# Performance work log

Hardware: AMD Instinct MI355X
Metric: run time of the kernel (lower is better)

The kernel has to match this reference:

```python
import jax, jax.numpy as jnp
import numpy as np

EPS = 1e-5

def layer_norm(x, g, b):
    m = jnp.mean(x, axis=-1, keepdims=True)
    v = jnp.var(x, axis=-1, keepdims=True)
    return (x - m) / jnp.sqrt(v + EPS) * g + b

def setup_inputs() -> dict:
    key = jax.random.key(0)
    B, N, D, H, F = 2, 2048, 1024, 16, 4096
    ks = jax.random.split(key, 12)
    s = 0.02
    return {
        "x": jax.random.normal(ks[0], (B, N, D), dtype=jnp.float32),
        "wq": jax.random.normal(ks[1], (D, D), dtype=jnp.float32) * s,
        "bq": jnp.zeros((D,), jnp.float32),
        "wk": jax.random.normal(ks[2], (D, D), dtype=jnp.float32) * s,
        "bk": jnp.zeros((D,), jnp.float32),
        "wv": jax.random.normal(ks[3], (D, D), dtype=jnp.float32) * s,
        "bv": jnp.zeros((D,), jnp.float32),
        "g1": jnp.ones((D,), jnp.float32),
        "b1": jnp.zeros((D,), jnp.float32),
        "g2": jnp.ones((D,), jnp.float32),
        "b2": jnp.zeros((D,), jnp.float32),
        "w1": jax.random.normal(ks[4], (D, F), dtype=jnp.float32) * s,
        "bw1": jnp.zeros((F,), jnp.float32),
        "gf": jnp.ones((F,), jnp.float32),
        "bf": jnp.zeros((F,), jnp.float32),
        "w2": jax.random.normal(ks[5], (F, D), dtype=jnp.float32) * s,
        "bw2": jnp.zeros((D,), jnp.float32),
        "num_heads": 16,
    }

def reference(x, wq, bq, wk, bk, wv, bv, g1, b1, g2, b2, w1, bw1, gf, bf, w2, bw2, num_heads):
    B, N, D = x.shape
    H = num_heads
    E = D // H
    h = layer_norm(x, g1, b1)
    q = (h @ wq + bq).reshape(B, N, H, E).transpose(0, 2, 1, 3)  # B H N E
    k = (h @ wk + bk).reshape(B, N, H, E).transpose(0, 2, 1, 3)
    v = (h @ wv + bv).reshape(B, N, H, E).transpose(0, 2, 1, 3)
    # NOTE: original scales by 1/sqrt(1/emb_dim) == sqrt(emb_dim)
    scale = jnp.sqrt(jnp.float32(D))
    score = jnp.einsum('bhne,bhme->bhnm', q, k) * scale  # B H N N
    w = jax.nn.softmax(score, axis=-1)
    attn = jnp.einsum('bhnm,bhme->bhne', w, v)
    attn = attn.transpose(0, 2, 1, 3).reshape(B, N, D)
    x = x + attn  # dropout = identity in eval
    h2 = layer_norm(x, g2, b2)
    # MLP: Linear -> (Dropout) -> LayerNorm -> ReLU -> Linear; NO residual add (faithful to source)
    u = layer_norm(h2 @ w1 + bw1, gf, bf)
    return jax.nn.relu(u) @ w2 + bw2
```

## Files before the change

### kernel.cpp

```cpp
#include <hip/hip_runtime.h>

typedef unsigned short u16;
typedef _Float16 f16;
typedef _Float16 f16x8 __attribute__((ext_vector_type(8)));
typedef float f32x4 __attribute__((ext_vector_type(4)));
typedef unsigned short u16x4 __attribute__((ext_vector_type(4)));
typedef unsigned int u32x4 __attribute__((ext_vector_type(4)));

__device__ __forceinline__ u16 f2h(float f) {
    f16 h = (f16)f;
    return *reinterpret_cast<u16*>(&h);
}
__device__ __forceinline__ float h2f(u16 u) {
    f16 h = *reinterpret_cast<f16*>(&u);
    return (float)h;
}

__device__ __forceinline__ float exp2v(float x) { return __builtin_amdgcn_exp2f(x); }

__device__ __forceinline__ unsigned cvtpkh(float lo, float hi) {
    unsigned r;
    asm("v_cvt_pkrtz_f16_f32 %0, %1, %2" : "=v"(r) : "v"(lo), "v"(hi));
    return r;
}

__device__ __forceinline__ void gload16(const u16* g, u16* l) {
    __builtin_amdgcn_global_load_lds((const __attribute__((address_space(1))) unsigned int*)g,
                                     (__attribute__((address_space(3))) unsigned int*)l, 16, 0, 0);
}

#define RAW_BARRIER() __builtin_amdgcn_s_barrier()
#define WAITCNT_VM(N) asm volatile("s_waitcnt vmcnt(" #N ")" ::: "memory")

__device__ __forceinline__ int xcd_swz(int bid, int nwg) {
    return (bid & 7) * (nwg >> 3) + (bid >> 3);
}

__global__ void transpose_cast3(const float* __restrict__ W0, u16* __restrict__ T0,
                                const float* __restrict__ W1, u16* __restrict__ T1,
                                const float* __restrict__ W2, u16* __restrict__ T2,
                                int K, int N) {
    __shared__ float t[32][33];
    const float* W = (blockIdx.z == 0) ? W0 : (blockIdx.z == 1) ? W1 : W2;
    u16* Wt = (blockIdx.z == 0) ? T0 : (blockIdx.z == 1) ? T1 : T2;
    const int n0 = blockIdx.x * 32, k0 = blockIdx.y * 32;
    const int tx = threadIdx.x, ty = threadIdx.y;
#pragma unroll
    for (int i = 0; i < 32; i += 8)
        t[ty + i][tx] = W[(size_t)(k0 + ty + i) * N + n0 + tx];
    __syncthreads();
#pragma unroll
    for (int i = 0; i < 32; i += 8)
        Wt[(size_t)(n0 + ty + i) * K + k0 + tx] = f2h(t[tx][ty + i]);
}

__global__ void transpose_cast(const float* __restrict__ W, u16* __restrict__ Wt,
                               int K, int N) {
    __shared__ float t[32][33];
    const int n0 = blockIdx.x * 32, k0 = blockIdx.y * 32;
    const int tx = threadIdx.x, ty = threadIdx.y;
#pragma unroll
    for (int i = 0; i < 32; i += 8)
        t[ty + i][tx] = W[(size_t)(k0 + ty + i) * N + n0 + tx];
    __syncthreads();
#pragma unroll
    for (int i = 0; i < 32; i += 8)
        Wt[(size_t)(n0 + ty + i) * K + k0 + tx] = f2h(t[tx][ty + i]);
}

__global__ __launch_bounds__(256) void ln_f32_f16(const float* __restrict__ in,
                                                  const float* __restrict__ g,
                                                  const float* __restrict__ b,
                                                  u16* __restrict__ out) {
    constexpr int Dl = 1024;
    const int row = blockIdx.x, tid = threadIdx.x;
    const float4 v = *(const float4*)&in[(size_t)row * Dl + tid * 4];
    const float* vp = (const float*)&v;
    float s = v.x + v.y + v.z + v.w;
    float s2 = v.x * v.x + v.y * v.y + v.z * v.z + v.w * v.w;
#pragma unroll
    for (int off = 32; off; off >>= 1) { s += __shfl_xor(s, off); s2 += __shfl_xor(s2, off); }
    __shared__ float red[8];
    const int lane = tid & 63, wid = tid >> 6;
    if (lane == 0) { red[wid] = s; red[4 + wid] = s2; }
    __syncthreads();
    s = red[0] + red[1] + red[2] + red[3];
    s2 = red[4] + red[5] + red[6] + red[7];
    const float mean = s * (1.0f / Dl);
    const float rstd = rsqrtf(s2 * (1.0f / Dl) - mean * mean + 1e-5f);
    u16x4 pk;
#pragma unroll
    for (int i = 0; i < 4; ++i) {
        const int col = tid * 4 + i;
        pk[i] = f2h((vp[i] - mean) * rstd * g[col] + b[col]);
    }
    *(u16x4*)&out[(size_t)row * Dl + tid * 4] = pk;
}

__global__ __launch_bounds__(256) void ln_relu_f16(u16* __restrict__ mid,
                                                   const float* __restrict__ g,
                                                   const float* __restrict__ b) {
    constexpr int Fl = 4096;
    const int row = blockIdx.x, tid = threadIdx.x;
    u16* rp = mid + (size_t)row * Fl;
    float v[16];
    u32x4 raw[2];
#pragma unroll
    for (int c = 0; c < 2; ++c) raw[c] = *(const u32x4*)&rp[tid * 16 + c * 8];
#pragma unroll
    for (int c = 0; c < 2; ++c)
#pragma unroll
        for (int j = 0; j < 4; ++j) {
            const unsigned u = raw[c][j];
            v[c * 8 + j * 2] = h2f((u16)(u & 0xffffu));
            v[c * 8 + j * 2 + 1] = h2f((u16)(u >> 16));
        }
    float s = 0.f, s2 = 0.f;
#pragma unroll
    for (int i = 0; i < 16; ++i) { s += v[i]; s2 += v[i] * v[i]; }
#pragma unroll
    for (int off = 32; off; off >>= 1) { s += __shfl_xor(s, off); s2 += __shfl_xor(s2, off); }
    __shared__ float red[8];
    const int lane = tid & 63, wid = tid >> 6;
    if (lane == 0) { red[wid] = s; red[4 + wid] = s2; }
    __syncthreads();
    s = red[0] + red[1] + red[2] + red[3];
    s2 = red[4] + red[5] + red[6] + red[7];
    const float mean = s * (1.0f / Fl);
    const float rstd = rsqrtf(s2 * (1.0f / Fl) - mean * mean + 1e-5f);
    unsigned w[8];
#pragma unroll
    for (int j = 0; j < 8; ++j) {
        const int col = tid * 16 + j * 2;
        const float y0 = fmaxf((v[j * 2] - mean) * rstd * g[col] + b[col], 0.f);
        const float y1 = fmaxf((v[j * 2 + 1] - mean) * rstd * g[col + 1] + b[col + 1], 0.f);
        w[j] = (unsigned)f2h(y0) | ((unsigned)f2h(y1) << 16);
    }
    *(u32x4*)&rp[tid * 16] = *(u32x4*)&w[0];
    *(u32x4*)&rp[tid * 16 + 8] = *(u32x4*)&w[4];
}

template <int EPI, int BN>
__global__ __launch_bounds__(256, 2) void gemm_f16(const u16* __restrict__ A,
                                                   const u16* __restrict__ Bt,
                                                   const float* __restrict__ bias,
                                                   u16* __restrict__ outB,
                                                   float* __restrict__ outF,
                                                   int M_, int N_, int K_) {
    constexpr int BK = 32;
    constexpr int NJ = BN / 32;
    __shared__ u16 As[2][128 * BK];
    __shared__ u16 Bs[2][BN * BK];
    const int tid = threadIdx.x;
    const int lane = tid & 63;
    const int wid = tid >> 6;
    const int nM = gridDim.y;
    const int swz = xcd_swz(blockIdx.y * gridDim.x + blockIdx.x, gridDim.x * gridDim.y);
    const int m0 = (swz % nM) * 128;
    const int n0 = (swz / nM) * BN;
    const int wr = (wid >> 1) * 64;
    const int wc = (wid & 1) * (BN / 2);
    const int fr = lane & 15;
    const int fg = (lane >> 4) * 8;

    const int srow = wid * 32 + (lane >> 2);
    const int srB = wid * (BN / 4) + (lane >> 2);
    const int scol = (lane & 3) * 8;
    const u16* pa0 = A + (size_t)(m0 + srow) * K_ + scol;
    const u16* pa1 = pa0 + (size_t)16 * K_;
    const u16* pb0 = Bt + (size_t)(n0 + srB) * K_ + scol;
    const u16* pb1 = pb0 + (size_t)16 * K_;
    const int aoff = wid * 1024;
    const int boff = wid * (BN / 4) * BK;

    auto stage = [&](int k0, int buf) {
        gload16(pa0 + k0, &As[buf][aoff]);
        gload16(pa1 + k0, &As[buf][aoff + 512]);
        gload16(pb0 + k0, &Bs[buf][boff]);
        if constexpr (BN == 128) gload16(pb1 + k0, &Bs[buf][boff + 512]);
    };

    f32x4 acc[4][NJ] = {};
    const int nt = K_ / BK;

    stage(0, 0);
    WAITCNT_VM(0);
    RAW_BARRIER();

    for (int t = 0; t < nt; ++t) {
        const int buf = t & 1;
        if (t + 1 < nt) stage((t + 1) * BK, buf ^ 1);
        f16x8 aF[4], bF[NJ];
#pragma unroll
        for (int i = 0; i < 4; ++i) aF[i] = *(const f16x8*)&As[buf][(wr + i * 16 + fr) * BK + fg];
#pragma unroll
        for (int j = 0; j < NJ; ++j) bF[j] = *(const f16x8*)&Bs[buf][(wc + j * 16 + fr) * BK + fg];
#pragma unroll
        for (int i = 0; i < 4; ++i)
#pragma unroll
            for (int j = 0; j < NJ; ++j)
                acc[i][j] = __builtin_amdgcn_mfma_f32_16x16x32_f16(aF[i], bF[j], acc[i][j], 0, 0, 0);
        WAITCNT_VM(0);
        RAW_BARRIER();
    }

    const int g4 = (lane >> 4) * 4;
#pragma unroll
    for (int i = 0; i < 4; ++i) {
#pragma unroll
        for (int j = 0; j < NJ; ++j) {
            const int mb = m0 + wr + i * 16 + g4;
            const int nb = n0 + wc + j * 16 + fr;
            const float bv = bias[nb];
#pragma unroll
            for (int r = 0; r < 4; ++r)
                outB[(size_t)(mb + r) * N_ + nb] = f2h(acc[i][j][r] + bv);
        }
    }
}

__global__ __launch_bounds__(256, 4) void gemm_f16_splitk(const u16* __restrict__ A,
                                                          const u16* __restrict__ Bt,
                                                          float* __restrict__ p0,
                                                          float* __restrict__ p1,
                                                          int M_, int N_, int K_) {
    constexpr int BK = 32, BN = 64;
    __shared__ u16 As[2][128 * BK];
    __shared__ u16 Bs[2][BN * BK];
    const int tid = threadIdx.x;
    const int lane = tid & 63;
    const int wid = tid >> 6;
    const int nM = gridDim.y;
    const int swz = xcd_swz(blockIdx.y * gridDim.x + blockIdx.x, gridDim.x * gridDim.y);
    const int m0 = (swz % nM) * 128;
    const int n0 = (swz / nM) * BN;
    const int kBase = blockIdx.z * (K_ >> 1);
    float* dst = blockIdx.z ? p1 : p0;
    const int wr = (wid >> 1) * 64;
    const int wc = (wid & 1) * (BN / 2);
    const int fr = lane & 15;
    const int fg = (lane >> 4) * 8;

    const int srow = wid * 32 + (lane >> 2);
    const int srB = wid * (BN / 4) + (lane >> 2);
    const int scol = (lane & 3) * 8;
    const u16* pa0 = A + (size_t)(m0 + srow) * K_ + kBase + scol;
    const u16* pa1 = pa0 + (size_t)16 * K_;
    const u16* pb0 = Bt + (size_t)(n0 + srB) * K_ + kBase + scol;
    const u16* pb1 = pb0 + (size_t)16 * K_;
    const int aoff = wid * 1024;
    const int boff = wid * (BN / 4) * BK;

    auto stage = [&](int k0, int buf) {
        gload16(pa0 + k0, &As[buf][aoff]);
        gload16(pa1 + k0, &As[buf][aoff + 512]);
        gload16(pb0 + k0, &Bs[buf][boff]);
    };

    f32x4 acc[4][2] = {};
    const int nt = (K_ >> 1) / BK;

    stage(0, 0);
    WAITCNT_VM(0);
    RAW_BARRIER();

    for (int t = 0; t < nt; ++t) {
        const int buf = t & 1;
        if (t + 1 < nt) stage((t + 1) * BK, buf ^ 1);
        f16x8 aF[4], bF[2];
#pragma unroll
        for (int i = 0; i < 4; ++i) aF[i] = *(const f16x8*)&As[buf][(wr + i * 16 + fr) * BK + fg];
#pragma unroll
        for (int j = 0; j < 2; ++j) bF[j] = *(const f16x8*)&Bs[buf][(wc + j * 16 + fr) * BK + fg];
#pragma unroll
        for (int i = 0; i < 4; ++i)
#pragma unroll
            for (int j = 0; j < 2; ++j)
                acc[i][j] = __builtin_amdgcn_mfma_f32_16x16x32_f16(aF[i], bF[j], acc[i][j], 0, 0, 0);
        WAITCNT_VM(0);
        RAW_BARRIER();
    }

    const int g4 = (lane >> 4) * 4;
#pragma unroll
    for (int i = 0; i < 4; ++i)
#pragma unroll
        for (int j = 0; j < 2; ++j) {
            const int mb = m0 + wr + i * 16 + g4;
            const int nb = n0 + wc + j * 16 + fr;
#pragma unroll
            for (int r = 0; r < 4; ++r)
                dst[(size_t)(mb + r) * N_ + nb] = acc[i][j][r];
        }
}

__global__ __launch_bounds__(256) void reduce2_bias(const float* __restrict__ p0,
                                                    const float* __restrict__ p1,
                                                    const float* __restrict__ bias,
                                                    float* __restrict__ out, int N_) {
    const size_t i4 = (size_t)blockIdx.x * 256 + threadIdx.x;
    const float4 a = ((const float4*)p0)[i4];
    const float4 b = ((const float4*)p1)[i4];
    const int col4 = (int)(i4 % (N_ / 4));
    const float4 bi = ((const float4*)bias)[col4];
    float4 o;
    o.x = a.x + b.x + bi.x;
    o.y = a.y + b.y + bi.y;
    o.z = a.z + b.z + bi.z;
    o.w = a.w + b.w + bi.w;
    ((float4*)out)[i4] = o;
}

__global__ __launch_bounds__(256, 4) void gemm_qkv(const u16* __restrict__ A,
                                                   const u16* __restrict__ qW,
                                                   const u16* __restrict__ kW,
                                                   const u16* __restrict__ vW,
                                                   const float* __restrict__ bq,
                                                   const float* __restrict__ bk,
                                                   const float* __restrict__ bv,
                                                   u16* __restrict__ qb, u16* __restrict__ kb,
                                                   u16* __restrict__ vtb,
                                                   int M_, int K_) {
    constexpr int BK = 32;
    __shared__ u16 As[2][128 * BK];
    __shared__ u16 Bs[2][64 * BK];
    const int tid = threadIdx.x;
    const int lane = tid & 63;
    const int wid = tid >> 6;
    const int nM = gridDim.y;
    const int swz = xcd_swz(blockIdx.y * gridDim.x + blockIdx.x, gridDim.x * gridDim.y);
    const int m0 = (swz % nM) * 128;
    const int bx = swz / nM;
    const int region = bx >> 4;
    const int n0 = (bx & 15) * 64;
    const int wr = (wid >> 1) * 64;
    const int wc = (wid & 1) * 32;
    const int fr = lane & 15;
    const int fg = (lane >> 4) * 8;

    const int srow = wid * 32 + (lane >> 2);
    const int srB = wid * 16 + (lane >> 2);
    const int scol = (lane & 3) * 8;

    const u16* B = (region == 0) ? qW : (region == 1) ? kW : vW;
    const u16* pa0 = A + (size_t)(m0 + srow) * K_ + scol;
    const u16* pa1 = pa0 + (size_t)16 * K_;
    const u16* pb = B + (size_t)(n0 + srB) * K_ + scol;
    const int aoff = wid * 1024;
    const int boff = wid * 512;

    auto stage = [&](int k0, int buf) {
        gload16(pa0 + k0, &As[buf][aoff]);
        gload16(pa1 + k0, &As[buf][aoff + 512]);
        gload16(pb + k0, &Bs[buf][boff]);
    };

    f32x4 acc[4][2] = {};
    const int nt = K_ / BK;

    stage(0, 0);
    WAITCNT_VM(0);
    RAW_BARRIER();

    for (int t = 0; t < nt; ++t) {
        const int buf = t & 1;
        if (t + 1 < nt) stage((t + 1) * BK, buf ^ 1);
        f16x8 aF[4], bF[2];
#pragma unroll
        for (int i = 0; i < 4; ++i) aF[i] = *(const f16x8*)&As[buf][(wr + i * 16 + fr) * BK + fg];
#pragma unroll
        for (int j = 0; j < 2; ++j) bF[j] = *(const f16x8*)&Bs[buf][(wc + j * 16 + fr) * BK + fg];
#pragma unroll
        for (int i = 0; i < 4; ++i)
#pragma unroll
            for (int j = 0; j < 2; ++j)
                acc[i][j] = __builtin_amdgcn_mfma_f32_16x16x32_f16(aF[i], bF[j], acc[i][j], 0, 0, 0);
        WAITCNT_VM(0);
        RAW_BARRIER();
    }

    const float* bias = (region == 0) ? bq : (region == 1) ? bk : bv;
    const float scale = (region == 0) ? 32.f : 1.f;
    const int g4 = (lane >> 4) * 4;
#pragma unroll
    for (int i = 0; i < 4; ++i) {
#pragma unroll
        for (int j = 0; j < 2; ++j) {
            const int mb = m0 + wr + i * 16 + g4;
            const int nb = n0 + wc + j * 16 + fr;
            const float bv_ = bias[nb];
            const int h = nb >> 6, e = nb & 63;
            if (region < 2) {
                u16* outp = (region == 0) ? qb : kb;
#pragma unroll
                for (int r = 0; r < 4; ++r) {
                    const int m = mb + r;
                    const size_t idx = ((size_t)((m >> 11) * 16 + h) * 2048 + (m & 2047)) * 64 + e;
                    outp[idx] = f2h((acc[i][j][r] + bv_) * scale);
                }
            } else {
                const int b_ = mb >> 11, np = mb & 2047;
                u16x4 pk;
#pragma unroll
                for (int r = 0; r < 4; ++r) pk[r] = f2h(acc[i][j][r] + bv_);
                *(u16x4*)&vtb[((size_t)(b_ * 16 + h) * 64 + e) * 2048 + np] = pk;
            }
        }
    }
}

__global__ __launch_bounds__(512, 4) void attn_kernel(const u16* __restrict__ q,
                                                      const u16* __restrict__ k,
                                                      const u16* __restrict__ vt,
                                                      const float* __restrict__ x,
                                                      float* __restrict__ x2) {
    constexpr int N = 2048, E = 64, KB = 64, NT = N / KB;
    constexpr float L2E = 1.4426950408889634f;
    __shared__ u16 Ks[2][64 * 64];
    __shared__ u16 Vs[2][64 * 64];
    __shared__ unsigned Ps[8][16][36];

    const int tid = threadIdx.x;
    const int lane = tid & 63;
    const int wid = tid >> 6;
    const int swzb = xcd_swz(blockIdx.x, gridDim.x);
    const int bh = swzb >> 4;
    const int q0 = (swzb & 15) * 128;
    const u16* qh = q + (size_t)bh * N * E;
    const u16* kh = k + (size_t)bh * N * E;
    const u16* vh = vt + (size_t)bh * E * N;

    const int fr = lane & 15;
    const int fgrp = lane >> 4;
    const int fg8 = fgrp * 8;
    int pc[2];
#pragma unroll
    for (int ks = 0; ks < 2; ++ks) pc[ks] = 8 * (((ks << 2) + fgrp) ^ (fr & 7));

    const int srow = wid * 8 + (lane >> 3);
    const int swc = 8 * ((lane & 7) ^ (lane >> 3));
    u16* dK = &Ks[0][wid * 8 * 64];
    u16* dV = &Vs[0][wid * 8 * 64];
    constexpr int BUFO = 64 * 64;

    f16x8 qf[2];
#pragma unroll
    for (int ks = 0; ks < 2; ++ks)
        qf[ks] = *(const f16x8*)&qh[(size_t)(q0 + wid * 16 + fr) * E + ks * 32 + fg8];

    auto stage = [&](int t, int buf) {
        const size_t kb = (size_t)t * KB;
        gload16(kh + (kb + srow) * E + swc, dK + buf * BUFO);
        gload16(vh + (size_t)srow * N + kb + swc, dV + buf * BUFO);
    };

    f32x4 o[4] = {};
    float mrow = -1e30f, lpart = 0.f;

    stage(0, 0);

    for (int t = 0; t < NT; ++t) {
        const int buf = t & 1;
        RAW_BARRIER();
        if (t + 1 < NT) {
            stage(t + 1, buf ^ 1);
            WAITCNT_VM(2);
        } else {
            WAITCNT_VM(0);
        }
        RAW_BARRIER();

        const u16* KK = &Ks[buf][0];
        const u16* VV = &Vs[buf][0];

        f32x4 s[4] = {};
        __builtin_amdgcn_s_setprio(1);
#pragma unroll
        for (int fn = 0; fn < 4; ++fn)
#pragma unroll
            for (int ks = 0; ks < 2; ++ks) {
                const f16x8 kf = *(const f16x8*)&KK[(fn * 16 + fr) * 64 + pc[ks]];
                s[fn] = __builtin_amdgcn_mfma_f32_16x16x32_f16(kf, qf[ks], s[fn], 0, 0, 0);
            }
        __builtin_amdgcn_s_setprio(0);

        float lmax = fmaxf(fmaxf(fmaxf(s[0][0], s[0][1]), fmaxf(s[0][2], s[0][3])),
                           fmaxf(fmaxf(s[1][0], s[1][1]), fmaxf(s[1][2], s[1][3])));
        lmax = fmaxf(lmax, fmaxf(fmaxf(fmaxf(s[2][0], s[2][1]), fmaxf(s[2][2], s[2][3])),
                                 fmaxf(fmaxf(s[3][0], s[3][1]), fmaxf(s[3][2], s[3][3]))));
        if (!__all(lmax <= mrow + 8.f)) {
            float m2 = fmaxf(lmax, __shfl_xor(lmax, 16));
            m2 = fmaxf(m2, __shfl_xor(m2, 32));
            const float mnew = fmaxf(mrow, m2);
            const float fac = exp2v((mrow - mnew) * L2E);
            mrow = mnew;
            lpart *= fac;
            float fo[4];
#pragma unroll
            for (int r = 0; r < 4; ++r) fo[r] = __shfl(fac, fgrp * 4 + r);
#pragma unroll
            for (int fe = 0; fe < 4; ++fe)
#pragma unroll
                for (int r = 0; r < 4; ++r) o[fe][r] *= fo[r];
        }

        const float nml = -mrow * L2E;
#pragma unroll
        for (int fn = 0; fn < 4; ++fn) {
            const float p0 = exp2v(fmaf(s[fn][0], L2E, nml));
            const float p1 = exp2v(fmaf(s[fn][1], L2E, nml));
            const float p2 = exp2v(fmaf(s[fn][2], L2E, nml));
            const float p3 = exp2v(fmaf(s[fn][3], L2E, nml));
            lpart += (p0 + p1) + (p2 + p3);
            uint2 w;
            w.x = cvtpkh(p0, p1);
            w.y = cvtpkh(p2, p3);
            *(uint2*)&Ps[wid][fr][fn * 8 + fgrp * 2] = w;
        }

        const u16* prow = (const u16*)&Ps[wid][fr][0];
        f16x8 pf[2];
#pragma unroll
        for (int ks = 0; ks < 2; ++ks) pf[ks] = *(const f16x8*)&prow[ks * 32 + fg8];
        __builtin_amdgcn_s_setprio(1);
#pragma unroll
        for (int fe = 0; fe < 4; ++fe)
#pragma unroll
            for (int ks = 0; ks < 2; ++ks) {
                const f16x8 vf = *(const f16x8*)&VV[(fe * 16 + fr) * 64 + pc[ks]];
                o[fe] = __builtin_amdgcn_mfma_f32_16x16x32_f16(pf[ks], vf, o[fe], 0, 0, 0);
            }
        __builtin_amdgcn_s_setprio(0);
    }

    float lsum = lpart + __shfl_xor(lpart, 16);
    lsum += __shfl_xor(lsum, 32);
    float rl[4];
#pragma unroll
    for (int r = 0; r < 4; ++r) rl[r] = 1.0f / __shfl(lsum, fgrp * 4 + r);

    const int b_ = bh >> 4, h_ = bh & 15;
#pragma unroll
    for (int fe = 0; fe < 4; ++fe)
#pragma unroll
        for (int r = 0; r < 4; ++r) {
            const int npos = q0 + wid * 16 + fgrp * 4 + r;
            const size_t idx = ((size_t)(b_ * 2048 + npos)) * 1024 + h_ * 64 + fe * 16 + fr;
            x2[idx] = x[idx] + o[fe][r] * rl[r];
        }
}

extern "C" void kernel_launch(void* const* d_in, const int* in_sizes, int n_in,
                              void* d_out, int out_size, void* d_ws, size_t ws_size,
                              hipStream_t stream) {
    const float* x = (const float*)d_in[0];
    const float* wq = (const float*)d_in[1];
    const float* bq = (const float*)d_in[2];
    const float* wk = (const float*)d_in[3];
    const float* bk = (const float*)d_in[4];
    const float* wv = (const float*)d_in[5];
    const float* bv = (const float*)d_in[6];
    const float* g1 = (const float*)d_in[7];
    const float* b1 = (const float*)d_in[8];
    const float* g2 = (const float*)d_in[9];
    const float* b2 = (const float*)d_in[10];
    const float* w1 = (const float*)d_in[11];
    const float* bw1 = (const float*)d_in[12];
    const float* gf = (const float*)d_in[13];
    const float* bf = (const float*)d_in[14];
    const float* w2 = (const float*)d_in[15];
    const float* bw2 = (const float*)d_in[16];
    float* out = (float*)d_out;

    constexpr int Bc = 2, Nc = 2048, Dc = 1024, Fc = 4096, Mc = 4096;

    char* ws = (char*)d_ws;
    auto alloc = [&](size_t bytes) {
        char* p = ws;
        ws += (bytes + 255) & ~(size_t)255;
        return p;
    };
    u16* wqt = (u16*)alloc((size_t)Dc * Dc * 2);
    u16* wkt = (u16*)alloc((size_t)Dc * Dc * 2);
    u16* wvt = (u16*)alloc((size_t)Dc * Dc * 2);
    u16* w1t = (u16*)alloc((size_t)Dc * Fc * 2);
    u16* w2t = (u16*)alloc((size_t)Fc * Dc * 2);
    char* region = (char*)alloc((size_t)Mc * Dc * 2 * 4);
    u16* h1 = (u16*)region;
    u16* qb = h1 + (size_t)Mc * Dc;
    u16* kb = qb + (size_t)Mc * Dc;
    u16* vtb = kb + (size_t)Mc * Dc;
    u16* mid = (u16*)region;
    float* x2 = (float*)alloc((size_t)Mc * Dc * 4);
    u16* h2 = (u16*)alloc((size_t)Mc * Dc * 2);
    float* p1 = (float*)alloc((size_t)Mc * Dc * 4);
    float* p0 = x2;

    const dim3 tb(32, 8);
    transpose_cast3<<<dim3(Dc / 32, Dc / 32, 3), tb, 0, stream>>>(wq, wqt, wk, wkt, wv, wvt, Dc, Dc);
    transpose_cast<<<dim3(Fc / 32, Dc / 32), tb, 0, stream>>>(w1, w1t, Dc, Fc);
    transpose_cast<<<dim3(Dc / 32, Fc / 32), tb, 0, stream>>>(w2, w2t, Fc, Dc);

    ln_f32_f16<<<Mc, 256, 0, stream>>>(x, g1, b1, h1);

    gemm_qkv<<<dim3(48, Mc / 128), 256, 0, stream>>>(h1, wqt, wkt, wvt, bq, bk, bv,
                                                     qb, kb, vtb, Mc, Dc);

    attn_kernel<<<Bc * 16 * (Nc / 128), 512, 0, stream>>>(qb, kb, vtb, x, x2);

    ln_f32_f16<<<Mc, 256, 0, stream>>>(x2, g2, b2, h2);

    gemm_f16<0, 128><<<dim3(Fc / 128, Mc / 128), 256, 0, stream>>>(h2, w1t, bw1, mid, nullptr, Mc, Fc, Dc);

    ln_relu_f16<<<Mc, 256, 0, stream>>>(mid, gf, bf);

    gemm_f16_splitk<<<dim3(Dc / 64, Mc / 128, 2), 256, 0, stream>>>(mid, w2t, p0, p1, Mc, Dc, Fc);
    reduce2_bias<<<(Mc * Dc) / 1024, 256, 0, stream>>>(p0, p1, bw2, out, Dc);
}
```

Baseline: 261.8 us.

## Swizzle LDS tile layout in GEMMs, reorder block mapping, raise occupancy

Applies an XOR swizzle to the 16-byte column chunk in both the global-to-LDS staging offset and the fragment read offset of the three GEMM kernels, to cut LDS bank conflicts on the MFMA operand loads. It also changes the swizzled block-to-tile mapping from M-major to N-major ordering, which alters L2 reuse, and raises the launch-bounds occupancy hint of gemm_f16 from 2 to 4 blocks per CU, which tightens the register budget. An fp32 output epilogue for the non-zero EPI variant is added too. The swizzle has to line up exactly between writer and reader lanes, or the results are wrong.

```diff
diff --git a/kernel.cpp b/kernel.cpp
--- a/kernel.cpp
+++ b/kernel.cpp
@@ -141,7 +141,7 @@
 }
 
 template <int EPI, int BN>
-__global__ __launch_bounds__(256, 2) void gemm_f16(const u16* __restrict__ A,
+__global__ __launch_bounds__(256, 4) void gemm_f16(const u16* __restrict__ A,
                                                    const u16* __restrict__ Bt,
                                                    const float* __restrict__ bias,
                                                    u16* __restrict__ outB,
@@ -154,18 +154,17 @@
     const int tid = threadIdx.x;
     const int lane = tid & 63;
     const int wid = tid >> 6;
-    const int nM = gridDim.y;
     const int swz = xcd_swz(blockIdx.y * gridDim.x + blockIdx.x, gridDim.x * gridDim.y);
-    const int m0 = (swz % nM) * 128;
-    const int n0 = (swz / nM) * BN;
+    const int m0 = (swz / gridDim.x) * 128;
+    const int n0 = (swz % gridDim.x) * BN;
     const int wr = (wid >> 1) * 64;
     const int wc = (wid & 1) * (BN / 2);
     const int fr = lane & 15;
-    const int fg = (lane >> 4) * 8;
+    const int fg = 8 * ((lane >> 4) ^ ((fr >> 1) & 3));
 
     const int srow = wid * 32 + (lane >> 2);
     const int srB = wid * (BN / 4) + (lane >> 2);
-    const int scol = (lane & 3) * 8;
+    const int scol = 8 * ((lane & 3) ^ ((lane >> 3) & 3));
     const u16* pa0 = A + (size_t)(m0 + srow) * K_ + scol;
     const u16* pa1 = pa0 + (size_t)16 * K_;
     const u16* pb0 = Bt + (size_t)(n0 + srB) * K_ + scol;
@@ -212,9 +211,15 @@
             const int mb = m0 + wr + i * 16 + g4;
             const int nb = n0 + wc + j * 16 + fr;
             const float bv = bias[nb];
-#pragma unroll
-            for (int r = 0; r < 4; ++r)
-                outB[(size_t)(mb + r) * N_ + nb] = f2h(acc[i][j][r] + bv);
+            if constexpr (EPI == 0) {
+#pragma unroll
+                for (int r = 0; r < 4; ++r)
+                    outB[(size_t)(mb + r) * N_ + nb] = f2h(acc[i][j][r] + bv);
+            } else {
+#pragma unroll
+                for (int r = 0; r < 4; ++r)
+                    outF[(size_t)(mb + r) * N_ + nb] = acc[i][j][r] + bv;
+            }
         }
     }
 }
@@ -230,24 +235,22 @@
     const int tid = threadIdx.x;
     const int lane = tid & 63;
     const int wid = tid >> 6;
-    const int nM = gridDim.y;
     const int swz = xcd_swz(blockIdx.y * gridDim.x + blockIdx.x, gridDim.x * gridDim.y);
-    const int m0 = (swz % nM) * 128;
-    const int n0 = (swz / nM) * BN;
+    const int m0 = (swz / gridDim.x) * 128;
+    const int n0 = (swz % gridDim.x) * BN;
     const int kBase = blockIdx.z * (K_ >> 1);
     float* dst = blockIdx.z ? p1 : p0;
     const int wr = (wid >> 1) * 64;
     const int wc = (wid & 1) * (BN / 2);
     const int fr = lane & 15;
-    const int fg = (lane >> 4) * 8;
+    const int fg = 8 * ((lane >> 4) ^ ((fr >> 1) & 3));
 
     const int srow = wid * 32 + (lane >> 2);
     const int srB = wid * (BN / 4) + (lane >> 2);
-    const int scol = (lane & 3) * 8;
+    const int scol = 8 * ((lane & 3) ^ ((lane >> 3) & 3));
     const u16* pa0 = A + (size_t)(m0 + srow) * K_ + kBase + scol;
     const u16* pa1 = pa0 + (size_t)16 * K_;
     const u16* pb0 = Bt + (size_t)(n0 + srB) * K_ + kBase + scol;
-    const u16* pb1 = pb0 + (size_t)16 * K_;
     const int aoff = wid * 1024;
     const int boff = wid * (BN / 4) * BK;
 
@@ -327,20 +330,19 @@
     const int tid = threadIdx.x;
     const int lane = tid & 63;
     const int wid = tid >> 6;
-    const int nM = gridDim.y;
     const int swz = xcd_swz(blockIdx.y * gridDim.x + blockIdx.x, gridDim.x * gridDim.y);
-    const int m0 = (swz % nM) * 128;
-    const int bx = swz / nM;
+    const int bx = swz % gridDim.x;
     const int region = bx >> 4;
     const int n0 = (bx & 15) * 64;
+    const int m0 = (swz / gridDim.x) * 128;
     const int wr = (wid >> 1) * 64;
     const int wc = (wid & 1) * 32;
     const int fr = lane & 15;
-    const int fg = (lane >> 4) * 8;
+    const int fg = 8 * ((lane >> 4) ^ ((fr >> 1) & 3));
 
     const int srow = wid * 32 + (lane >> 2);
     const int srB = wid * 16 + (lane >> 2);
-    const int scol = (lane & 3) * 8;
+    const int scol = 8 * ((lane & 3) ^ ((lane >> 3) & 3));
 
     const u16* B = (region == 0) ? qW : (region == 1) ? kW : vW;
     const u16* pa0 = A + (size_t)(m0 + srow) * K_ + scol;
```

New measurement: 260.5 us (median of 2 runs). No clear change (-0.5%).
